# Kernel tuning notes

Measured on AMD Instinct MI355X. Metric: run time of the kernel, lower is better.

## Reference

```python
import jax, jax.numpy as jnp
import numpy as np

EPS = 1e-7  # perplexity log epsilon (matches compute_perplexity)


def _vq_step(carry, cb):
    """One QuantizeEMAReset layer (eval mode) applied to the current residual.

    carry: (residual (B,C,T), quantized_out (B,C,T)); cb: (K, C) codebook.
    """
    residual, quantized_out = carry
    B, C, T = residual.shape
    # preprocess: (B,C,T) -> (B*T, C)
    xf = jnp.transpose(residual, (0, 2, 1)).reshape(-1, C)
    dist = (jnp.sum(xf * xf, axis=1, keepdims=True)
            - 2.0 * (xf @ cb.T)
            + jnp.sum(cb * cb, axis=1))           # (B*T, K)
    idx = jnp.argmin(dist, axis=1)                # (B*T,)
    xd = cb[idx]                                  # dequantize gather (B*T, C)
    # commitment loss: mse(x, x_d.detach())
    commit = jnp.mean((xf - jax.lax.stop_gradient(xd)) ** 2)
    # perplexity from code-usage histogram
    counts = jnp.zeros((cb.shape[0],), xf.dtype).at[idx].add(1.0)
    prob = counts / xf.shape[0]
    perplexity = jnp.exp(-jnp.sum(prob * jnp.log(prob + EPS)))
    # straight-through estimator
    xd_st = xf + jax.lax.stop_gradient(xd - xf)
    quantized = jnp.transpose(xd_st.reshape(B, T, C), (0, 2, 1))  # (B,C,T)
    residual = residual - jax.lax.stop_gradient(quantized)
    quantized_out = quantized_out + quantized
    return (residual, quantized_out), (idx.reshape(B, T), commit, perplexity)


def _forward(x, codebooks):
    init = (x, jnp.zeros_like(x))
    (_, qout), (idxs, losses, perps) = jax.lax.scan(_vq_step, init, codebooks)
    all_indices = jnp.transpose(idxs, (1, 2, 0))  # (B, T, Q)
    return qout, all_indices, jnp.mean(losses), jnp.mean(perps)


def setup_inputs() -> dict:
    key = jax.random.key(0)
    kx, kc = jax.random.split(key)
    B, C, T = 64, 512, 256
    Q, K = 6, 1024
    x = jax.random.normal(kx, (B, C, T), dtype=jnp.float32)
    codebooks = jax.random.normal(kc, (Q, K, C), dtype=jnp.float32)
    return {"x": x, "codebooks": codebooks}


def reference(x, codebooks):
    # returns (quantized_out, all_indices, mean_commit_loss, mean_perplexity)
    return _forward(x, codebooks)
```

## Files before the change

kernel.cpp:

```cpp
#include <hip/hip_runtime.h>

typedef short bf16x8 __attribute__((ext_vector_type(8)));
typedef float f32x4  __attribute__((ext_vector_type(4)));

#define NB   64
#define NT   256
#define NC   512
#define NK   1024
#define NQ   6
#define NROWS (NB*NT)
#define QOUT_ELEMS 8388608
#define IDX_ELEMS  98304
#define DELTA 0.5f
#define CAP  64

#define WS_CAND   0
#define WS_CCNT   0x800000
#define WS_BIDX   0x810000
#define WS_COUNTS 0x820000
#define WS_CSUM   0x821000
#define WS_CMEAN  0x821020
#define WS_PERP   0x821040
#define WS_DONE   0x821060
#define WS_CBN    0x822000
#define WS_XHI    0x830000
#define WS_CBHI   (WS_XHI + 16777216)

__device__ __forceinline__ unsigned short f2bf(float f) {
    unsigned u = __float_as_uint(f);
    return (unsigned short)((u + 0x7FFFu + ((u >> 16) & 1u)) >> 16);
}

__device__ __forceinline__ void load_lds16(const unsigned short* g, unsigned short* l) {
    __builtin_amdgcn_global_load_lds(
        (const __attribute__((address_space(1))) unsigned int*)g,
        (__attribute__((address_space(3))) unsigned int*)l,
        16, 0, 0);
}

__device__ __forceinline__ unsigned lds_addr(const unsigned short* p) {
    return (unsigned)(unsigned long long)
        (const __attribute__((address_space(3))) unsigned short*)p;
}

#define DSR(d, b, IMM) \
    asm volatile("ds_read_b128 %0, %1 offset:" #IMM : "=v"(d) : "v"(b))

__global__ __launch_bounds__(256) void vq_cvt_cb(const float* __restrict__ cb,
                                                 unsigned short* __restrict__ cbhi,
                                                 float* __restrict__ cbn) {
    int lane = threadIdx.x & 63, wid = threadIdx.x >> 6;
    int code = blockIdx.x * 4 + wid;
    int layer = code >> 10, cin = code & 1023;
    const float* row = cb + (size_t)code * NC;
    float4 v0 = *(const float4*)(row + lane * 8);
    float4 v1 = *(const float4*)(row + lane * 8 + 4);
    float vs[8] = {v0.x, v0.y, v0.z, v0.w, v1.x, v1.y, v1.z, v1.w};
    ushort4 a, b;
    unsigned short* ap = &a.x; unsigned short* bp = &b.x;
    float s = 0.f;
    #pragma unroll
    for (int j = 0; j < 4; ++j) {
        s += vs[j] * vs[j] + vs[j+4] * vs[j+4];
        ap[j] = f2bf(vs[j]); bp[j] = f2bf(vs[j+4]);
    }
    size_t o = (size_t)layer * NK * NC
             + (((size_t)(lane >> 3) * NK + cin) << 6)
             + (((lane & 7) ^ (cin & 7)) << 3);
    *(ushort4*)(cbhi + o) = a; *(ushort4*)(cbhi + o + 4) = b;
    #pragma unroll
    for (int off = 32; off; off >>= 1) s += __shfl_down(s, off, 64);
    if (lane == 0) cbn[code] = 0.5f * s;
}

__global__ __launch_bounds__(256) void vq_cvt_x(const float* __restrict__ x,
                                                unsigned short* __restrict__ xh,
                                                unsigned int* __restrict__ candcnt,
                                                unsigned int* __restrict__ done) {
    __shared__ unsigned short hs[64][72];
    int bx = blockIdx.x;
    int b = bx >> 5, tt = (bx >> 3) & 3, kk = bx & 7;
    int c0 = kk << 6, t0 = tt << 6, tid = threadIdx.x;
    if (kk == 0 && tid < 64) candcnt[b * 256 + t0 + tid] = 0u;
    if (bx == 0 && tid == 0) *done = 0u;
    const float* base = x + (size_t)b * (NC * NT) + t0;
    #pragma unroll
    for (int i = 0; i < 4; ++i) {
        int f = tid + (i << 8);
        int c_l = f >> 4, t4 = f & 15;
        float4 v = *(const float4*)(base + (size_t)(c0 + c_l) * NT + (t4 << 2));
        ushort4 hh;
        hh.x = f2bf(v.x); hh.y = f2bf(v.y); hh.z = f2bf(v.z); hh.w = f2bf(v.w);
        *(ushort4*)&hs[c_l][t4 << 2] = hh;
    }
    __syncthreads();
    int row0 = b * NT + t0;
    #pragma unroll
    for (int i = 0; i < 4; ++i) {
        int f = tid + (i << 8);
        int r_l = f >> 4, c4 = f & 15;
        ushort4 hh;
        hh.x = hs[c4*4+0][r_l]; hh.y = hs[c4*4+1][r_l];
        hh.z = hs[c4*4+2][r_l]; hh.w = hs[c4*4+3][r_l];
        int cq = c4 >> 1, h = c4 & 1;
        *(ushort4*)(xh + (((size_t)kk * NROWS + row0 + r_l) << 6)
                       + ((cq ^ (r_l & 7)) << 3) + (h << 2)) = hh;
    }
}

__global__ __launch_bounds__(512, 2) void vq_dist(
    const unsigned short* __restrict__ xh, const unsigned short* __restrict__ ch,
    const float* __restrict__ cbn,
    unsigned int* __restrict__ cand, unsigned int* __restrict__ candcnt,
    unsigned int* __restrict__ counts, float* __restrict__ commit_slot)
{
    extern __shared__ unsigned short smem[];
    const int rb = blockIdx.x, cg = blockIdx.y, tid = threadIdx.x;
    if (rb == 0 && cg == 0) {
        for (int i = tid; i < NK; i += 512) counts[i] = 0u;
        if (tid == 0) *commit_slot = 0.f;
    }
    const int wave = tid >> 6, lane = tid & 63;
    const int idx16 = lane & 15, quad = lane >> 4;
    const int wm = wave >> 2, wn = wave & 3;
    const int m0 = rb * 256, n0 = cg * 256;

    const unsigned short* gsrc = (wave < 4) ? xh : ch;
    const int tbase = (wave < 4) ? m0 : n0;
    const size_t strideK = (size_t)((wave < 4) ? NROWS : NK) << 6;
    const unsigned short* gp = gsrc + ((size_t)tbase << 6) + ((wave & 3) << 12) + lane * 8;
    unsigned short* lp0 = &smem[((wave < 4) ? 0 : 16384) + ((wave & 3) << 12) + lane * 8];

    unsigned aB[2][2], bB[2][2];
    #pragma unroll
    for (int ks = 0; ks < 2; ++ks) {
        int slot = ((quad + 4 * ks) ^ (idx16 & 7)) << 3;
        aB[0][ks] = lds_addr(&smem[(wm * 128 + idx16) * 64 + slot]);
        bB[0][ks] = lds_addr(&smem[16384 + (wn * 64 + idx16) * 64 + slot]);
        aB[1][ks] = aB[0][ks] + 65536u;
        bB[1][ks] = bB[0][ks] + 65536u;
    }

    f32x4 acc[8][4];
    #pragma unroll
    for (int mt = 0; mt < 8; ++mt)
        #pragma unroll
        for (int nt = 0; nt < 4; ++nt) acc[mt][nt] = (f32x4){0.f, 0.f, 0.f, 0.f};

    #pragma unroll
    for (int i = 0; i < 8; ++i)
        load_lds16(gp + i * 512, lp0 + i * 512);

    #define KS_BODY(ABASE, BBASE)                                              \
    {                                                                          \
        bf16x8 a[8], b[4];                                                     \
        DSR(a[0], ABASE, 0);     DSR(a[1], ABASE, 2048);                       \
        DSR(a[2], ABASE, 4096);  DSR(a[3], ABASE, 6144);                       \
        DSR(a[4], ABASE, 8192);  DSR(a[5], ABASE, 10240);                      \
        DSR(a[6], ABASE, 12288); DSR(a[7], ABASE, 14336);                      \
        DSR(b[0], BBASE, 0);     DSR(b[1], BBASE, 2048);                       \
        DSR(b[2], BBASE, 4096);  DSR(b[3], BBASE, 6144);                       \
        asm volatile("s_waitcnt lgkmcnt(0)" ::: "memory");                     \
        __builtin_amdgcn_sched_barrier(0);                                     \
        __builtin_amdgcn_s_setprio(1);                                         \
        _Pragma("unroll")                                                      \
        for (int mt = 0; mt < 8; ++mt)                                         \
            _Pragma("unroll")                                                  \
            for (int nt = 0; nt < 4; ++nt)                                     \
                acc[mt][nt] = __builtin_amdgcn_mfma_f32_16x16x32_bf16(         \
                    a[mt], b[nt], acc[mt][nt], 0, 0, 0);                       \
        __builtin_amdgcn_s_setprio(0);                                         \
        __builtin_amdgcn_sched_barrier(0);                                     \
    }

    #pragma unroll
    for (int k = 0; k < 8; ++k) {
        const int BUF = k & 1;
        if (k < 7) {
            unsigned short* lp = lp0 + ((BUF ^ 1) << 15);
            const unsigned short* g = gp + (size_t)(k + 1) * strideK;
            #pragma unroll
            for (int i = 0; i < 8; ++i)
                load_lds16(g + i * 512, lp + i * 512);
            asm volatile("s_waitcnt vmcnt(8)" ::: "memory");
        } else {
            asm volatile("s_waitcnt vmcnt(0)" ::: "memory");
        }
        __builtin_amdgcn_s_barrier();
        __builtin_amdgcn_sched_barrier(0);
        KS_BODY(aB[BUF][0], bB[BUF][0]);
        KS_BODY(aB[BUF][1], bB[BUF][1]);
        __builtin_amdgcn_s_barrier();
        __builtin_amdgcn_sched_barrier(0);
    }
    #undef KS_BODY

    float cn[4]; int ng[4];
    #pragma unroll
    for (int nt = 0; nt < 4; ++nt) {
        ng[nt] = n0 + wn * 64 + nt * 16 + idx16;
        cn[nt] = cbn[ng[nt]];
    }
    #pragma unroll
    for (int mt = 0; mt < 8; ++mt) {
        #pragma unroll
        for (int r = 0; r < 4; ++r) {
            float sc[4];
            float m = 3.402823466e38f;
            #pragma unroll
            for (int nt = 0; nt < 4; ++nt) {
                sc[nt] = cn[nt] - acc[mt][nt][r];
                m = fminf(m, sc[nt]);
            }
            #pragma unroll
            for (int sft = 1; sft < 16; sft <<= 1)
                m = fminf(m, __shfl_xor(m, sft, 64));
            m += DELTA;
            const int row = m0 + wm * 128 + mt * 16 + quad * 4 + r;
            #pragma unroll
            for (int nt = 0; nt < 4; ++nt) {
                if (sc[nt] <= m) {
                    unsigned slot = atomicAdd(&candcnt[row], 1u);
                    if (slot < (unsigned)CAP)
                        ((uint2*)cand)[(size_t)row * CAP + slot] =
                            make_uint2((unsigned)ng[nt], __float_as_uint(sc[nt]));
                }
            }
        }
    }
}

__global__ __launch_bounds__(256) void vq_rescore(
    const float* __restrict__ src,
    const float* __restrict__ cb, const float* __restrict__ cbn,
    const unsigned int* __restrict__ cand, const unsigned int* __restrict__ candcnt,
    int* __restrict__ best_idx, float* __restrict__ out_idx,
    unsigned int* __restrict__ counts, int q)
{
    __shared__ float xl[16][512];
    const int tid = threadIdx.x;
    const int b = blockIdx.x >> 4, t0 = (blockIdx.x & 15) << 4;
    const float* base = src + (size_t)b * (NC * NT) + t0;
    #pragma unroll
    for (int i = 0; i < 8; ++i) {
        int f = tid + (i << 8);
        int c = f >> 2, t4 = f & 3;
        float4 v = *(const float4*)(base + (size_t)c * NT + (t4 << 2));
        xl[(t4 << 2) + 0][c] = v.x; xl[(t4 << 2) + 1][c] = v.y;
        xl[(t4 << 2) + 2][c] = v.z; xl[(t4 << 2) + 3][c] = v.w;
    }
    __syncthreads();
    const int w = tid >> 6, lane = tid & 63;
    const int row0 = b * NT + t0;
    const uint2* cp = (const uint2*)cand;
    for (int rr = 0; rr < 4; ++rr) {
        const int tl = w * 4 + rr;
        const int row = row0 + tl;
        float4 xa = *(const float4*)&xl[tl][lane << 3];
        float4 xb = *(const float4*)&xl[tl][(lane << 3) + 4];
        int n = (int)candcnt[row]; if (n > CAP) n = CAP;
        uint2 pr = make_uint2(0x7FFFFFFFu, 0x7F800000u);
        if (lane < n) pr = cp[(size_t)row * CAP + lane];
        float scf = __uint_as_float(pr.y);
        float rmin = scf;
        #pragma unroll
        for (int off = 1; off < 64; off <<= 1) rmin = fminf(rmin, __shfl_xor(rmin, off, 64));
        unsigned long long msk = __ballot(scf <= rmin + DELTA);
        float bs = 3.402823466e38f; int bi = 0x7FFFFFFF;
        while (msk) {
            int j = (int)__ffsll(msk) - 1; msk &= msk - 1;
            int code = __shfl((int)pr.x, j, 64);
            const float* cr = cb + (size_t)code * NC + (lane << 3);
            float4 ca = *(const float4*)cr;
            float4 cc = *(const float4*)(cr + 4);
            float s = xa.x*ca.x + xa.y*ca.y + xa.z*ca.z + xa.w*ca.w
                    + xb.x*cc.x + xb.y*cc.y + xb.z*cc.z + xb.w*cc.w;
            #pragma unroll
            for (int off = 1; off < 64; off <<= 1) s += __shfl_xor(s, off, 64);
            s = cbn[code] - s;
            if (s < bs || (s == bs && code < bi)) { bs = s; bi = code; }
        }
        if (lane == 0) {
            best_idx[row] = bi;
            out_idx[(size_t)row * NQ + q] = (float)bi;
            atomicAdd(&counts[bi], 1u);
        }
    }
}

__global__ __launch_bounds__(256) void vq_update(
    const float* __restrict__ src,
    float* __restrict__ dst,
    const float* __restrict__ x,
    const float* __restrict__ cb,
    const int* __restrict__ best_idx,
    unsigned short* __restrict__ xh,
    unsigned int* __restrict__ candcnt,
    unsigned int* __restrict__ counts,
    float* __restrict__ csum, float* __restrict__ cmean, float* __restrict__ perp,
    float* __restrict__ out_tail, unsigned int* __restrict__ done, int q)
{
    const int rb = blockIdx.x, tid = threadIdx.x;
    const int b = rb >> 2, t0 = (rb & 3) << 6;
    const int row0 = rb * 64;
    __shared__ int s_idx[64];
    __shared__ __align__(16) float qt[64][68];
    __shared__ float wsum[4];
    __shared__ unsigned int lastflag;
    if (tid < 64) {
        s_idx[tid] = best_idx[row0 + tid];
        candcnt[row0 + tid] = 0u;
    }
    __syncthreads();
    float cs = 0.f;
    const size_t base = (size_t)b * (NC * NT) + t0;
    for (int ct = 0; ct < 8; ++ct) {
        if (ct) __syncthreads();
        #pragma unroll
        for (int i = 0; i < 4; ++i) {
            int f = tid + (i << 8);
            int r = f >> 4, cf = f & 15;
            float4 v = *(const float4*)(cb + (size_t)s_idx[r] * NC + ct * 64 + (cf << 2));
            qt[(cf << 2) + 0][r] = v.x;
            qt[(cf << 2) + 1][r] = v.y;
            qt[(cf << 2) + 2][r] = v.z;
            qt[(cf << 2) + 3][r] = v.w;
        }
        __syncthreads();
        #pragma unroll
        for (int i = 0; i < 4; ++i) {
            int f = tid + (i << 8);
            int c_l = f >> 4, tf = f & 15;
            size_t o = base + (size_t)(ct * 64 + c_l) * NT + (tf << 2);
            float4 r4 = *(const float4*)(src + o);
            float4 q4 = *(const float4*)&qt[c_l][tf << 2];
            float4 n;
            n.x = r4.x - q4.x; n.y = r4.y - q4.y; n.z = r4.z - q4.z; n.w = r4.w - q4.w;
            float4 o4 = n;
            if (q == NQ - 1) {
                float4 xv = *(const float4*)(x + o);
                o4.x = xv.x - n.x; o4.y = xv.y - n.y;
                o4.z = xv.z - n.z; o4.w = xv.w - n.w;
            }
            *(float4*)(dst + o) = o4;
            *(float4*)&qt[c_l][tf << 2] = n;
            cs += n.x*n.x + n.y*n.y + n.z*n.z + n.w*n.w;
        }
        if (q < NQ - 1) {
            __syncthreads();
            #pragma unroll
            for (int i = 0; i < 4; ++i) {
                int f = tid + (i << 8);
                int r_l = f >> 4, c4 = f & 15;
                ushort4 hh;
                hh.x = f2bf(qt[c4*4+0][r_l]); hh.y = f2bf(qt[c4*4+1][r_l]);
                hh.z = f2bf(qt[c4*4+2][r_l]); hh.w = f2bf(qt[c4*4+3][r_l]);
                int cq = c4 >> 1, h = c4 & 1;
                *(ushort4*)(xh + (((size_t)ct * NROWS + row0 + r_l) << 6)
                               + ((cq ^ (r_l & 7)) << 3) + (h << 2)) = hh;
            }
        }
    }
    #pragma unroll
    for (int off = 32; off; off >>= 1) cs += __shfl_down(cs, off, 64);
    if ((tid & 63) == 0) wsum[tid >> 6] = cs;
    __syncthreads();
    if (tid == 0) {
        atomicAdd(&csum[q], wsum[0] + wsum[1] + wsum[2] + wsum[3]);
        __threadfence();
        lastflag = atomicAdd(done, 1u);
    }
    __syncthreads();
    if (lastflag == 255u) {
        float v = 0.f;
        for (int i = tid; i < NK; i += 256) {
            float p = (float)atomicAdd(&counts[i], 0u) * (1.f / (float)NROWS);
            v += p * logf(p + 1e-7f);
        }
        #pragma unroll
        for (int off = 32; off; off >>= 1) v += __shfl_down(v, off, 64);
        if ((tid & 63) == 0) wsum[tid >> 6] = v;
        __syncthreads();
        if (tid == 0) {
            float S = wsum[0] + wsum[1] + wsum[2] + wsum[3];
            perp[q]  = expf(-S);
            cmean[q] = atomicAdd(&csum[q], 0.f) * (1.f / ((float)NROWS * (float)NC));
            if (q == NQ - 1) {
                float mc = 0.f, mp = 0.f;
                for (int i = 0; i < NQ; ++i) { mc += cmean[i]; mp += perp[i]; }
                out_tail[0] = mc / (float)NQ;
                out_tail[1] = mp / (float)NQ;
            }
            *done = 0u;
        }
    }
}

extern "C" void kernel_launch(void* const* d_in, const int* in_sizes, int n_in,
                              void* d_out, int out_size, void* d_ws, size_t ws_size,
                              hipStream_t stream) {
    static int inited = 0;
    if (!inited) {
        (void)hipFuncSetAttribute((const void*)vq_dist,
                                  hipFuncAttributeMaxDynamicSharedMemorySize, 131072);
        inited = 1;
    }
    const float* x  = (const float*)d_in[0];
    const float* cb = (const float*)d_in[1];
    float* out      = (float*)d_out;
    float* res      = out;
    float* out_idx  = out + QOUT_ELEMS;
    float* out_tail = out + QOUT_ELEMS + IDX_ELEMS;
    char* ws = (char*)d_ws;
    unsigned int* cand    = (unsigned int*)(ws + WS_CAND);
    unsigned int* candcnt = (unsigned int*)(ws + WS_CCNT);
    int*          bidx    = (int*)(ws + WS_BIDX);
    unsigned int* counts  = (unsigned int*)(ws + WS_COUNTS);
    float* csum  = (float*)(ws + WS_CSUM);
    float* cmean = (float*)(ws + WS_CMEAN);
    float* perp  = (float*)(ws + WS_PERP);
    unsigned int* done = (unsigned int*)(ws + WS_DONE);
    float* cbn   = (float*)(ws + WS_CBN);
    unsigned short* xh   = (unsigned short*)(ws + WS_XHI);
    unsigned short* cbhi = (unsigned short*)(ws + WS_CBHI);

    vq_cvt_cb<<<1536, 256, 0, stream>>>(cb, cbhi, cbn);
    vq_cvt_x<<<2048, 256, 0, stream>>>(x, xh, candcnt, done);
    for (int q = 0; q < NQ; ++q) {
        const float* src = (q == 0) ? x : res;
        const float* cbq = cb + (size_t)q * NK * NC;
        vq_dist<<<dim3(64, 4), 512, 131072, stream>>>(
            xh, cbhi + (size_t)q * NK * NC, cbn + q * NK,
            cand, candcnt, counts, csum + q);
        vq_rescore<<<1024, 256, 0, stream>>>(src, cbq, cbn + q * NK, cand, candcnt,
                                             bidx, out_idx, counts, q);
        vq_update<<<256, 256, 0, stream>>>(src, res, x, cbq, bidx, xh, candcnt,
                                           counts, csum, cmean, perp, out_tail, done, q);
    }
}
```

Before: 766.7 us.

## Switch distance GEMM to int8 MFMA with per-code and per-tensor scales

Quantizes codebooks (per-code scale) and residuals (per-tensor scale from a running abs-max) to int8 and computes the candidate distances with i8 MFMA instead of bf16. It adds an abs-max reduction kernel, a 4-buffer load pipeline, and a new swizzle for the halved tile bytes. To cover the larger quantization error, the candidate margin is widened, and rows whose candidate list overflows fall back to an exact full scan over all codes. The wider margin and the possible full-scan fallback can add substantial rescore cost, and the 1.5x scale heuristic for later residual layers may clip values.

```diff
diff --git a/kernel.cpp b/kernel.cpp
--- a/kernel.cpp
+++ b/kernel.cpp
@@ -1,7 +1,7 @@
 #include <hip/hip_runtime.h>
 
-typedef short bf16x8 __attribute__((ext_vector_type(8)));
-typedef float f32x4  __attribute__((ext_vector_type(4)));
+typedef int   i32x4 __attribute__((ext_vector_type(4)));
+typedef float f32x4 __attribute__((ext_vector_type(4)));
 
 #define NB   64
 #define NT   256
@@ -11,7 +11,7 @@
 #define NROWS (NB*NT)
 #define QOUT_ELEMS 8388608
 #define IDX_ELEMS  98304
-#define DELTA 0.5f
+#define DELTA 10.0f
 #define CAP  64
 
 #define WS_CAND   0
@@ -22,184 +22,213 @@
 #define WS_CMEAN  0x821020
 #define WS_PERP   0x821040
 #define WS_DONE   0x821060
+#define WS_RMAX   0x821080
 #define WS_CBN    0x822000
+#define WS_CBS    0x828000
 #define WS_XHI    0x830000
-#define WS_CBHI   (WS_XHI + 16777216)
-
-__device__ __forceinline__ unsigned short f2bf(float f) {
-    unsigned u = __float_as_uint(f);
-    return (unsigned short)((u + 0x7FFFu + ((u >> 16) & 1u)) >> 16);
-}
-
-__device__ __forceinline__ void load_lds16(const unsigned short* g, unsigned short* l) {
+#define WS_CBHI   (WS_XHI + 8388608)
+
+#define KEY4(r) (((r) + ((r) >> 2)) & 3)
+
+__device__ __forceinline__ unsigned pack4i8(float a, float b, float c, float d, float is) {
+    int qa = (int)rintf(a * is), qb = (int)rintf(b * is);
+    int qc = (int)rintf(c * is), qd = (int)rintf(d * is);
+    qa = qa > 127 ? 127 : (qa < -127 ? -127 : qa);
+    qb = qb > 127 ? 127 : (qb < -127 ? -127 : qb);
+    qc = qc > 127 ? 127 : (qc < -127 ? -127 : qc);
+    qd = qd > 127 ? 127 : (qd < -127 ? -127 : qd);
+    return (qa & 0xff) | ((qb & 0xff) << 8) | ((qc & 0xff) << 16) | ((qd & 0xff) << 24);
+}
+
+__device__ __forceinline__ void load_lds16(const unsigned char* g, unsigned char* l) {
     __builtin_amdgcn_global_load_lds(
         (const __attribute__((address_space(1))) unsigned int*)g,
         (__attribute__((address_space(3))) unsigned int*)l,
         16, 0, 0);
 }
 
-__device__ __forceinline__ unsigned lds_addr(const unsigned short* p) {
+__device__ __forceinline__ unsigned lds_addr(const unsigned char* p) {
     return (unsigned)(unsigned long long)
-        (const __attribute__((address_space(3))) unsigned short*)p;
+        (const __attribute__((address_space(3))) unsigned char*)p;
 }
 
 #define DSR(d, b, IMM) \
     asm volatile("ds_read_b128 %0, %1 offset:" #IMM : "=v"(d) : "v"(b))
 
+__global__ __launch_bounds__(256) void vq_xmax(const float* __restrict__ x,
+                                               unsigned* __restrict__ rmax) {
+    __shared__ float wm[4];
+    const int tid = threadIdx.x;
+    float m = 0.f;
+    for (int i = blockIdx.x * 256 + tid; i < QOUT_ELEMS / 4; i += 1024 * 256) {
+        float4 v = ((const float4*)x)[i];
+        m = fmaxf(m, fmaxf(fmaxf(fabsf(v.x), fabsf(v.y)), fmaxf(fabsf(v.z), fabsf(v.w))));
+    }
+    #pragma unroll
+    for (int off = 32; off; off >>= 1) m = fmaxf(m, __shfl_down(m, off, 64));
+    if ((tid & 63) == 0) wm[tid >> 6] = m;
+    __syncthreads();
+    if (tid == 0)
+        atomicMax(rmax, __float_as_uint(fmaxf(fmaxf(wm[0], wm[1]), fmaxf(wm[2], wm[3]))));
+}
+
 __global__ __launch_bounds__(256) void vq_cvt_cb(const float* __restrict__ cb,
-                                                 unsigned short* __restrict__ cbhi,
-                                                 float* __restrict__ cbn) {
+                                                 unsigned char* __restrict__ cbhi,
+                                                 float* __restrict__ cbn,
+                                                 float* __restrict__ cbs) {
     int lane = threadIdx.x & 63, wid = threadIdx.x >> 6;
     int code = blockIdx.x * 4 + wid;
     int layer = code >> 10, cin = code & 1023;
     const float* row = cb + (size_t)code * NC;
     float4 v0 = *(const float4*)(row + lane * 8);
     float4 v1 = *(const float4*)(row + lane * 8 + 4);
-    float vs[8] = {v0.x, v0.y, v0.z, v0.w, v1.x, v1.y, v1.z, v1.w};
-    ushort4 a, b;
-    unsigned short* ap = &a.x; unsigned short* bp = &b.x;
-    float s = 0.f;
-    #pragma unroll
-    for (int j = 0; j < 4; ++j) {
-        s += vs[j] * vs[j] + vs[j+4] * vs[j+4];
-        ap[j] = f2bf(vs[j]); bp[j] = f2bf(vs[j+4]);
-    }
-    size_t o = (size_t)layer * NK * NC
-             + (((size_t)(lane >> 3) * NK + cin) << 6)
-             + (((lane & 7) ^ (cin & 7)) << 3);
-    *(ushort4*)(cbhi + o) = a; *(ushort4*)(cbhi + o + 4) = b;
+    float s = v0.x*v0.x + v0.y*v0.y + v0.z*v0.z + v0.w*v0.w
+            + v1.x*v1.x + v1.y*v1.y + v1.z*v1.z + v1.w*v1.w;
+    float am = fmaxf(fmaxf(fmaxf(fabsf(v0.x), fabsf(v0.y)), fmaxf(fabsf(v0.z), fabsf(v0.w))),
+                     fmaxf(fmaxf(fabsf(v1.x), fabsf(v1.y)), fmaxf(fabsf(v1.z), fabsf(v1.w))));
+    #pragma unroll
+    for (int off = 1; off < 64; off <<= 1) am = fmaxf(am, __shfl_xor(am, off, 64));
+    float is = 127.0f / am;
+    uint2 w;
+    w.x = pack4i8(v0.x, v0.y, v0.z, v0.w, is);
+    w.y = pack4i8(v1.x, v1.y, v1.z, v1.w, is);
+    int kk = lane >> 3, c8 = lane & 7, c16 = c8 >> 1, h = c8 & 1;
+    size_t o = (size_t)layer * (NK * NC) + (size_t)kk * (NK * 64) + (size_t)cin * 64
+             + (((unsigned)(c16 ^ KEY4(cin)) << 4) + (h << 3));
+    *(uint2*)(cbhi + o) = w;
     #pragma unroll
     for (int off = 32; off; off >>= 1) s += __shfl_down(s, off, 64);
-    if (lane == 0) cbn[code] = 0.5f * s;
+    if (lane == 0) { cbn[code] = 0.5f * s; cbs[code] = am * (1.0f / 127.0f); }
 }
 
 __global__ __launch_bounds__(256) void vq_cvt_x(const float* __restrict__ x,
-                                                unsigned short* __restrict__ xh,
+                                                unsigned char* __restrict__ xh,
                                                 unsigned int* __restrict__ candcnt,
-                                                unsigned int* __restrict__ done) {
-    __shared__ unsigned short hs[64][72];
+                                                unsigned int* __restrict__ done,
+                                                const unsigned* __restrict__ rmax) {
+    __shared__ float hs[64][68];
     int bx = blockIdx.x;
     int b = bx >> 5, tt = (bx >> 3) & 3, kk = bx & 7;
     int c0 = kk << 6, t0 = tt << 6, tid = threadIdx.x;
     if (kk == 0 && tid < 64) candcnt[b * 256 + t0 + tid] = 0u;
     if (bx == 0 && tid == 0) *done = 0u;
+    const float is = 127.0f / __uint_as_float(rmax[0]);
     const float* base = x + (size_t)b * (NC * NT) + t0;
     #pragma unroll
     for (int i = 0; i < 4; ++i) {
         int f = tid + (i << 8);
         int c_l = f >> 4, t4 = f & 15;
         float4 v = *(const float4*)(base + (size_t)(c0 + c_l) * NT + (t4 << 2));
-        ushort4 hh;
-        hh.x = f2bf(v.x); hh.y = f2bf(v.y); hh.z = f2bf(v.z); hh.w = f2bf(v.w);
-        *(ushort4*)&hs[c_l][t4 << 2] = hh;
+        *(float4*)&hs[c_l][t4 << 2] = v;
     }
     __syncthreads();
     int row0 = b * NT + t0;
-    #pragma unroll
-    for (int i = 0; i < 4; ++i) {
-        int f = tid + (i << 8);
-        int r_l = f >> 4, c4 = f & 15;
-        ushort4 hh;
-        hh.x = hs[c4*4+0][r_l]; hh.y = hs[c4*4+1][r_l];
-        hh.z = hs[c4*4+2][r_l]; hh.w = hs[c4*4+3][r_l];
-        int cq = c4 >> 1, h = c4 & 1;
-        *(ushort4*)(xh + (((size_t)kk * NROWS + row0 + r_l) << 6)
-                       + ((cq ^ (r_l & 7)) << 3) + (h << 2)) = hh;
-    }
+    int r_l = tid >> 2, c16 = tid & 3;
+    float v[16];
+    #pragma unroll
+    for (int j = 0; j < 16; ++j) v[j] = hs[c16 * 16 + j][r_l];
+    uint4 w;
+    w.x = pack4i8(v[0],  v[1],  v[2],  v[3],  is);
+    w.y = pack4i8(v[4],  v[5],  v[6],  v[7],  is);
+    w.z = pack4i8(v[8],  v[9],  v[10], v[11], is);
+    w.w = pack4i8(v[12], v[13], v[14], v[15], is);
+    *(uint4*)(xh + (((size_t)kk * NROWS + row0 + r_l) << 6)
+                 + ((unsigned)(c16 ^ KEY4(r_l)) << 4)) = w;
 }
 
 __global__ __launch_bounds__(512, 2) void vq_dist(
-    const unsigned short* __restrict__ xh, const unsigned short* __restrict__ ch,
-    const float* __restrict__ cbn,
+    const unsigned char* __restrict__ xh, const unsigned char* __restrict__ ch,
+    const float* __restrict__ cbn, const float* __restrict__ cbs,
+    const unsigned* __restrict__ rmax,
     unsigned int* __restrict__ cand, unsigned int* __restrict__ candcnt,
-    unsigned int* __restrict__ counts, float* __restrict__ commit_slot)
+    unsigned int* __restrict__ counts, float* __restrict__ commit_slot, int q)
 {
-    extern __shared__ unsigned short smem[];
+    extern __shared__ unsigned char smem[];
     const int rb = blockIdx.x, cg = blockIdx.y, tid = threadIdx.x;
     if (rb == 0 && cg == 0) {
         for (int i = tid; i < NK; i += 512) counts[i] = 0u;
         if (tid == 0) *commit_slot = 0.f;
     }
+    const float sx = ((q == 0) ? __uint_as_float(rmax[0])
+                               : 1.5f * __uint_as_float(rmax[q - 1])) * (1.0f / 127.0f);
     const int wave = tid >> 6, lane = tid & 63;
     const int idx16 = lane & 15, quad = lane >> 4;
     const int wm = wave >> 2, wn = wave & 3;
     const int m0 = rb * 256, n0 = cg * 256;
 
-    const unsigned short* gsrc = (wave < 4) ? xh : ch;
+    const unsigned char* gsrc = (wave < 4) ? xh : ch;
     const int tbase = (wave < 4) ? m0 : n0;
     const size_t strideK = (size_t)((wave < 4) ? NROWS : NK) << 6;
-    const unsigned short* gp = gsrc + ((size_t)tbase << 6) + ((wave & 3) << 12) + lane * 8;
-    unsigned short* lp0 = &smem[((wave < 4) ? 0 : 16384) + ((wave & 3) << 12) + lane * 8];
-
-    unsigned aB[2][2], bB[2][2];
-    #pragma unroll
-    for (int ks = 0; ks < 2; ++ks) {
-        int slot = ((quad + 4 * ks) ^ (idx16 & 7)) << 3;
-        aB[0][ks] = lds_addr(&smem[(wm * 128 + idx16) * 64 + slot]);
-        bB[0][ks] = lds_addr(&smem[16384 + (wn * 64 + idx16) * 64 + slot]);
-        aB[1][ks] = aB[0][ks] + 65536u;
-        bB[1][ks] = bB[0][ks] + 65536u;
-    }
-
-    f32x4 acc[8][4];
+    const unsigned char* gp = gsrc + ((size_t)(tbase + ((wave & 3) << 6)) << 6) + lane * 16;
+    unsigned char* lp0 = &smem[((wave < 4) ? 0 : 16384) + ((wave & 3) << 12) + lane * 16];
+
+    const unsigned slot = (unsigned)((quad ^ KEY4(idx16)) << 4);
+    const unsigned aB0 = lds_addr(&smem[(wm * 128 + idx16) * 64]) + slot;
+    const unsigned bB0 = lds_addr(&smem[16384 + (wn * 64 + idx16) * 64]) + slot;
+
+    i32x4 acc[8][4];
     #pragma unroll
     for (int mt = 0; mt < 8; ++mt)
         #pragma unroll
-        for (int nt = 0; nt < 4; ++nt) acc[mt][nt] = (f32x4){0.f, 0.f, 0.f, 0.f};
-
-    #pragma unroll
-    for (int i = 0; i < 8; ++i)
-        load_lds16(gp + i * 512, lp0 + i * 512);
-
-    #define KS_BODY(ABASE, BBASE)                                              \
-    {                                                                          \
-        bf16x8 a[8], b[4];                                                     \
-        DSR(a[0], ABASE, 0);     DSR(a[1], ABASE, 2048);                       \
-        DSR(a[2], ABASE, 4096);  DSR(a[3], ABASE, 6144);                       \
-        DSR(a[4], ABASE, 8192);  DSR(a[5], ABASE, 10240);                      \
-        DSR(a[6], ABASE, 12288); DSR(a[7], ABASE, 14336);                      \
-        DSR(b[0], BBASE, 0);     DSR(b[1], BBASE, 2048);                       \
-        DSR(b[2], BBASE, 4096);  DSR(b[3], BBASE, 6144);                       \
-        asm volatile("s_waitcnt lgkmcnt(0)" ::: "memory");                     \
-        __builtin_amdgcn_sched_barrier(0);                                     \
-        __builtin_amdgcn_s_setprio(1);                                         \
-        _Pragma("unroll")                                                      \
-        for (int mt = 0; mt < 8; ++mt)                                         \
-            _Pragma("unroll")                                                  \
-            for (int nt = 0; nt < 4; ++nt)                                     \
-                acc[mt][nt] = __builtin_amdgcn_mfma_f32_16x16x32_bf16(         \
-                    a[mt], b[nt], acc[mt][nt], 0, 0, 0);                       \
-        __builtin_amdgcn_s_setprio(0);                                         \
-        __builtin_amdgcn_sched_barrier(0);                                     \
-    }
+        for (int nt = 0; nt < 4; ++nt) acc[mt][nt] = (i32x4){0, 0, 0, 0};
+
+    #define STAGE(KK) {                                                        \
+        const unsigned char* g = gp + (size_t)(KK) * strideK;                  \
+        unsigned char* lp = lp0 + (((KK) & 3) << 15);                          \
+        load_lds16(g,        lp);        load_lds16(g + 1024, lp + 1024);      \
+        load_lds16(g + 2048, lp + 2048); load_lds16(g + 3072, lp + 3072); }
+
+    STAGE(0); STAGE(1); STAGE(2);
 
     #pragma unroll
     for (int k = 0; k < 8; ++k) {
-        const int BUF = k & 1;
-        if (k < 7) {
-            unsigned short* lp = lp0 + ((BUF ^ 1) << 15);
-            const unsigned short* g = gp + (size_t)(k + 1) * strideK;
-            #pragma unroll
-            for (int i = 0; i < 8; ++i)
-                load_lds16(g + i * 512, lp + i * 512);
+        if (k < 5) {
+            STAGE(k + 3);
+            asm volatile("s_waitcnt vmcnt(12)" ::: "memory");
+        } else if (k == 5) {
             asm volatile("s_waitcnt vmcnt(8)" ::: "memory");
+        } else if (k == 6) {
+            asm volatile("s_waitcnt vmcnt(4)" ::: "memory");
         } else {
             asm volatile("s_waitcnt vmcnt(0)" ::: "memory");
         }
         __builtin_amdgcn_s_barrier();
         __builtin_amdgcn_sched_barrier(0);
-        KS_BODY(aB[BUF][0], bB[BUF][0]);
-        KS_BODY(aB[BUF][1], bB[BUF][1]);
+        {
+            const unsigned boff = (unsigned)((k & 3) << 15);
+            const unsigned ab = aB0 + boff, bb = bB0 + boff;
+            union { i32x4 v; long l[2]; } a[8], b[4];
+            DSR(a[0].v, ab, 0);    DSR(a[1].v, ab, 1024);
+            DSR(a[2].v, ab, 2048); DSR(a[3].v, ab, 3072);
+            DSR(a[4].v, ab, 4096); DSR(a[5].v, ab, 5120);
+            DSR(a[6].v, ab, 6144); DSR(a[7].v, ab, 7168);
+            DSR(b[0].v, bb, 0);    DSR(b[1].v, bb, 1024);
+            DSR(b[2].v, bb, 2048); DSR(b[3].v, bb, 3072);
+            asm volatile("s_waitcnt lgkmcnt(0)" ::: "memory");
+            __builtin_amdgcn_sched_barrier(0);
+            __builtin_amdgcn_s_setprio(1);
+            #pragma unroll
+            for (int h = 0; h < 2; ++h)
+                #pragma unroll
+                for (int mt = 0; mt < 8; ++mt)
+                    #pragma unroll
+                    for (int nt = 0; nt < 4; ++nt)
+                        acc[mt][nt] = __builtin_amdgcn_mfma_i32_16x16x32_i8(
+                            a[mt].l[h], b[nt].l[h], acc[mt][nt], 0, 0, 0);
+            __builtin_amdgcn_s_setprio(0);
+            __builtin_amdgcn_sched_barrier(0);
+        }
         __builtin_amdgcn_s_barrier();
         __builtin_amdgcn_sched_barrier(0);
     }
-    #undef KS_BODY
-
-    float cn[4]; int ng[4];
+    #undef STAGE
+
+    float cn[4], sl[4]; int ng[4];
     #pragma unroll
     for (int nt = 0; nt < 4; ++nt) {
         ng[nt] = n0 + wn * 64 + nt * 16 + idx16;
         cn[nt] = cbn[ng[nt]];
+        sl[nt] = sx * cbs[ng[nt]];
     }
     #pragma unroll
     for (int mt = 0; mt < 8; ++mt) {
@@ -209,7 +238,7 @@
             float m = 3.402823466e38f;
             #pragma unroll
             for (int nt = 0; nt < 4; ++nt) {
-                sc[nt] = cn[nt] - acc[mt][nt][r];
+                sc[nt] = cn[nt] - sl[nt] * (float)acc[mt][nt][r];
                 m = fminf(m, sc[nt]);
             }
             #pragma unroll
@@ -220,9 +249,9 @@
             #pragma unroll
             for (int nt = 0; nt < 4; ++nt) {
                 if (sc[nt] <= m) {
-                    unsigned slot = atomicAdd(&candcnt[row], 1u);
-                    if (slot < (unsigned)CAP)
-                        ((uint2*)cand)[(size_t)row * CAP + slot] =
+                    unsigned slot2 = atomicAdd(&candcnt[row], 1u);
+                    if (slot2 < (unsigned)CAP)
+                        ((uint2*)cand)[(size_t)row * CAP + slot2] =
                             make_uint2((unsigned)ng[nt], __float_as_uint(sc[nt]));
                 }
             }
@@ -258,27 +287,41 @@
         const int row = row0 + tl;
         float4 xa = *(const float4*)&xl[tl][lane << 3];
         float4 xb = *(const float4*)&xl[tl][(lane << 3) + 4];
-        int n = (int)candcnt[row]; if (n > CAP) n = CAP;
-        uint2 pr = make_uint2(0x7FFFFFFFu, 0x7F800000u);
-        if (lane < n) pr = cp[(size_t)row * CAP + lane];
-        float scf = __uint_as_float(pr.y);
-        float rmin = scf;
-        #pragma unroll
-        for (int off = 1; off < 64; off <<= 1) rmin = fminf(rmin, __shfl_xor(rmin, off, 64));
-        unsigned long long msk = __ballot(scf <= rmin + DELTA);
+        int n = (int)candcnt[row];
         float bs = 3.402823466e38f; int bi = 0x7FFFFFFF;
-        while (msk) {
-            int j = (int)__ffsll(msk) - 1; msk &= msk - 1;
-            int code = __shfl((int)pr.x, j, 64);
-            const float* cr = cb + (size_t)code * NC + (lane << 3);
-            float4 ca = *(const float4*)cr;
-            float4 cc = *(const float4*)(cr + 4);
-            float s = xa.x*ca.x + xa.y*ca.y + xa.z*ca.z + xa.w*ca.w
-                    + xb.x*cc.x + xb.y*cc.y + xb.z*cc.z + xb.w*cc.w;
-            #pragma unroll
-            for (int off = 1; off < 64; off <<= 1) s += __shfl_xor(s, off, 64);
-            s = cbn[code] - s;
-            if (s < bs || (s == bs && code < bi)) { bs = s; bi = code; }
+        if (n > CAP) {
+            for (int code = 0; code < NK; ++code) {
+                const float* cr = cb + (size_t)code * NC + (lane << 3);
+                float4 ca = *(const float4*)cr;
+                float4 cc = *(const float4*)(cr + 4);
+                float s = xa.x*ca.x + xa.y*ca.y + xa.z*ca.z + xa.w*ca.w
+                        + xb.x*cc.x + xb.y*cc.y + xb.z*cc.z + xb.w*cc.w;
+                #pragma unroll
+                for (int off = 1; off < 64; off <<= 1) s += __shfl_xor(s, off, 64);
+                s = cbn[code] - s;
+                if (s < bs || (s == bs && code < bi)) { bs = s; bi = code; }
+            }
+        } else {
+            uint2 pr = make_uint2(0x7FFFFFFFu, 0x7F800000u);
+            if (lane < n) pr = cp[(size_t)row * CAP + lane];
+            float scf = __uint_as_float(pr.y);
+            float rmin = scf;
+            #pragma unroll
+            for (int off = 1; off < 64; off <<= 1) rmin = fminf(rmin, __shfl_xor(rmin, off, 64));
+            unsigned long long msk = __ballot(scf <= rmin + DELTA);
+            while (msk) {
+                int j = (int)__ffsll(msk) - 1; msk &= msk - 1;
+                int code = __shfl((int)pr.x, j, 64);
+                const float* cr = cb + (size_t)code * NC + (lane << 3);
+                float4 ca = *(const float4*)cr;
+                float4 cc = *(const float4*)(cr + 4);
+                float s = xa.x*ca.x + xa.y*ca.y + xa.z*ca.z + xa.w*ca.w
+                        + xb.x*cc.x + xb.y*cc.y + xb.z*cc.z + xb.w*cc.w;
+                #pragma unroll
+                for (int off = 1; off < 64; off <<= 1) s += __shfl_xor(s, off, 64);
+                s = cbn[code] - s;
+                if (s < bs || (s == bs && code < bi)) { bs = s; bi = code; }
+            }
         }
         if (lane == 0) {
             best_idx[row] = bi;
@@ -294,7 +337,8 @@
     const float* __restrict__ x,
     const float* __restrict__ cb,
     const int* __restrict__ best_idx,
-    unsigned short* __restrict__ xh,
+    unsigned char* __restrict__ xh,
+    unsigned* __restrict__ rmax,
     unsigned int* __restrict__ candcnt,
     unsigned int* __restrict__ counts,
     float* __restrict__ csum, float* __restrict__ cmean, float* __restrict__ perp,
@@ -305,14 +349,16 @@
     const int row0 = rb * 64;
     __shared__ int s_idx[64];
     __shared__ __align__(16) float qt[64][68];
-    __shared__ float wsum[4];
+    __shared__ float wsum[4], wmax[4];
     __shared__ unsigned int lastflag;
     if (tid < 64) {
         s_idx[tid] = best_idx[row0 + tid];
         candcnt[row0 + tid] = 0u;
     }
-    __syncthreads();
-    float cs = 0.f;
+    const float emit_is = (q < NQ - 1)
+        ? 127.0f / (1.5f * __uint_as_float(rmax[q])) : 0.f;
+    __syncthreads();
+    float cs = 0.f, am = 0.f;
     const size_t base = (size_t)b * (NC * NT) + t0;
     for (int ct = 0; ct < 8; ++ct) {
         if (ct) __syncthreads();
@@ -345,27 +391,35 @@
             *(float4*)(dst + o) = o4;
             *(float4*)&qt[c_l][tf << 2] = n;
             cs += n.x*n.x + n.y*n.y + n.z*n.z + n.w*n.w;
+            am = fmaxf(am, fmaxf(fmaxf(fabsf(n.x), fabsf(n.y)),
+                                 fmaxf(fabsf(n.z), fabsf(n.w))));
         }
         if (q < NQ - 1) {
             __syncthreads();
-            #pragma unroll
-            for (int i = 0; i < 4; ++i) {
-                int f = tid + (i << 8);
-                int r_l = f >> 4, c4 = f & 15;
-                ushort4 hh;
-                hh.x = f2bf(qt[c4*4+0][r_l]); hh.y = f2bf(qt[c4*4+1][r_l]);
-                hh.z = f2bf(qt[c4*4+2][r_l]); hh.w = f2bf(qt[c4*4+3][r_l]);
-                int cq = c4 >> 1, h = c4 & 1;
-                *(ushort4*)(xh + (((size_t)ct * NROWS + row0 + r_l) << 6)
-                               + ((cq ^ (r_l & 7)) << 3) + (h << 2)) = hh;
-            }
-        }
-    }
-    #pragma unroll
-    for (int off = 32; off; off >>= 1) cs += __shfl_down(cs, off, 64);
-    if ((tid & 63) == 0) wsum[tid >> 6] = cs;
+            int r_l = tid >> 2, c16 = tid & 3;
+            float v[16];
+            #pragma unroll
+            for (int j = 0; j < 16; ++j) v[j] = qt[c16 * 16 + j][r_l];
+            uint4 w;
+            w.x = pack4i8(v[0],  v[1],  v[2],  v[3],  emit_is);
+            w.y = pack4i8(v[4],  v[5],  v[6],  v[7],  emit_is);
+            w.z = pack4i8(v[8],  v[9],  v[10], v[11], emit_is);
+            w.w = pack4i8(v[12], v[13], v[14], v[15], emit_is);
+            *(uint4*)(xh + (((size_t)ct * NROWS + row0 + r_l) << 6)
+                         + ((unsigned)(c16 ^ KEY4(r_l)) << 4)) = w;
+        }
+    }
+    #pragma unroll
+    for (int off = 32; off; off >>= 1) {
+        cs += __shfl_down(cs, off, 64);
+        am = fmaxf(am, __shfl_down(am, off, 64));
+    }
+    if ((tid & 63) == 0) { wsum[tid >> 6] = cs; wmax[tid >> 6] = am; }
     __syncthreads();
     if (tid == 0) {
+        if (q < NQ - 1)
+            atomicMax(&rmax[q + 1], __float_as_uint(
+                fmaxf(fmaxf(wmax[0], wmax[1]), fmaxf(wmax[2], wmax[3]))));
         atomicAdd(&csum[q], wsum[0] + wsum[1] + wsum[2] + wsum[3]);
         __threadfence();
         lastflag = atomicAdd(done, 1u);
@@ -420,21 +474,25 @@
     float* cmean = (float*)(ws + WS_CMEAN);
     float* perp  = (float*)(ws + WS_PERP);
     unsigned int* done = (unsigned int*)(ws + WS_DONE);
+    unsigned* rmax = (unsigned*)(ws + WS_RMAX);
     float* cbn   = (float*)(ws + WS_CBN);
-    unsigned short* xh   = (unsigned short*)(ws + WS_XHI);
-    unsigned short* cbhi = (unsigned short*)(ws + WS_CBHI);
-
-    vq_cvt_cb<<<1536, 256, 0, stream>>>(cb, cbhi, cbn);
-    vq_cvt_x<<<2048, 256, 0, stream>>>(x, xh, candcnt, done);
+    float* cbs   = (float*)(ws + WS_CBS);
+    unsigned char* xh   = (unsigned char*)(ws + WS_XHI);
+    unsigned char* cbhi = (unsigned char*)(ws + WS_CBHI);
+
+    hipMemsetAsync(ws + WS_RMAX, 0, 32, stream);
+    vq_xmax<<<1024, 256, 0, stream>>>(x, rmax);
+    vq_cvt_cb<<<1536, 256, 0, stream>>>(cb, cbhi, cbn, cbs);
+    vq_cvt_x<<<2048, 256, 0, stream>>>(x, xh, candcnt, done, rmax);
     for (int q = 0; q < NQ; ++q) {
         const float* src = (q == 0) ? x : res;
         const float* cbq = cb + (size_t)q * NK * NC;
         vq_dist<<<dim3(64, 4), 512, 131072, stream>>>(
-            xh, cbhi + (size_t)q * NK * NC, cbn + q * NK,
-            cand, candcnt, counts, csum + q);
+            xh, cbhi + (size_t)q * (NK * NC), cbn + q * NK, cbs + q * NK, rmax,
+            cand, candcnt, counts, csum + q, q);
         vq_rescore<<<1024, 256, 0, stream>>>(src, cbq, cbn + q * NK, cand, candcnt,
                                              bidx, out_idx, counts, q);
-        vq_update<<<256, 256, 0, stream>>>(src, res, x, cbq, bidx, xh, candcnt,
+        vq_update<<<256, 256, 0, stream>>>(src, res, x, cbq, bidx, xh, rmax, candcnt,
                                            counts, csum, cmean, perp, out_tail, done, q);
     }
 }
```

After: 1.261 ms. 64.5% more time.
